# Kernel optimization log

Measured on AMD Instinct MI355X. Metric: run time of the kernel, lower is better.

The kernel has to match this reference:

```python
import jax, jax.numpy as jnp
import numpy as np

B = 32          # batch_size (scenes)
P_PER_B = 256   # proposals per scene (max_n_proposals, equal by construction)
N = B * P_PER_B # total proposals = 8192
PTS = 1024      # points per proposal
M = 128         # cfg.m, instance feature dim
LANG = 256      # lang_size
H = 128         # hidden_size
EPS = 1e-5      # BatchNorm eps


def setup_inputs() -> dict:
    key = jax.random.key(0)
    ks = jax.random.split(key, 16)
    feats = jax.random.normal(ks[0], (N, M), jnp.float32)
    total_pts = N * PTS
    # proposals_idx: (total_pts, 2) = [proposal_id, global_point_id]; points are
    # contiguous per proposal, proposals contiguous per scene.
    prop_ids = jnp.repeat(jnp.arange(N, dtype=jnp.int32), PTS)
    pt_ids = jnp.arange(total_pts, dtype=jnp.int32)
    proposals_idx = jnp.stack([prop_ids, pt_ids], axis=1)
    proposals_offset = jnp.arange(N + 1, dtype=jnp.int32) * PTS
    b_offsets = jnp.arange(B + 1, dtype=jnp.int32) * (P_PER_B * PTS)
    lang_emb = jax.random.normal(ks[1], (B, LANG), jnp.float32)
    # parameters: fuse = Conv1d(LANG+M -> H, k=1) + ReLU
    W_fuse = jax.random.normal(ks[2], (H, LANG + M), jnp.float32) * 0.05
    b_fuse = jnp.zeros((H,), jnp.float32)
    # match = Conv1d(H,H,1)+ReLU+BN, Conv1d(H,H,1)+ReLU+BN, Conv1d(H,1,1)
    W1 = jax.random.normal(ks[3], (H, H), jnp.float32) * 0.05
    b1 = jnp.zeros((H,), jnp.float32)
    g1 = jnp.ones((H,), jnp.float32)
    be1 = jnp.zeros((H,), jnp.float32)
    rm1 = jax.random.normal(ks[4], (H,), jnp.float32) * 0.1
    rv1 = jax.random.uniform(ks[5], (H,), jnp.float32, 0.5, 1.5)
    W2 = jax.random.normal(ks[6], (H, H), jnp.float32) * 0.05
    b2 = jnp.zeros((H,), jnp.float32)
    g2 = jnp.ones((H,), jnp.float32)
    be2 = jnp.zeros((H,), jnp.float32)
    rm2 = jax.random.normal(ks[7], (H,), jnp.float32) * 0.1
    rv2 = jax.random.uniform(ks[8], (H,), jnp.float32, 0.5, 1.5)
    W3 = jax.random.normal(ks[9], (1, H), jnp.float32) * 0.05
    b3 = jnp.zeros((1,), jnp.float32)
    return {
        'aggregated_vote_features': feats,
        'proposals_idx': proposals_idx,
        'proposals_offset': proposals_offset,
        'b_offsets': b_offsets,
        'lang_emb': lang_emb,
        'W_fuse': W_fuse, 'b_fuse': b_fuse,
        'W1': W1, 'b1': b1, 'g1': g1, 'be1': be1, 'rm1': rm1, 'rv1': rv1,
        'W2': W2, 'b2': b2, 'g2': g2, 'be2': be2, 'rm2': rm2, 'rv2': rv2,
        'W3': W3, 'b3': b3,
    }


def _bn(x, g, be, rm, rv):
    # eval-mode BatchNorm1d over channel dim of (B, C, P)
    scale = g / jnp.sqrt(rv + EPS)
    return (x - rm[None, :, None]) * scale[None, :, None] + be[None, :, None]


def reference(aggregated_vote_features, proposals_idx, proposals_offset, b_offsets,
              lang_emb, W_fuse, b_fuse, W1, b1, g1, be1, rm1, rv1,
              W2, b2, g2, be2, rm2, rv2, W3, b3):
    # --- vectorized replacement of the host-sync batch-id loop ---
    first_pts = proposals_idx[proposals_offset[:-1], 1]            # (N,) first point of each proposal
    bid = jnp.searchsorted(b_offsets, first_pts, side='right') - 1  # (N,) proposal_batch_ids
    # --- ragged -> padded gather (vectorized scatter by per-batch position) ---
    counts = jax.ops.segment_sum(jnp.ones_like(bid), bid, num_segments=B)
    offs = jnp.concatenate([jnp.zeros((1,), counts.dtype), jnp.cumsum(counts)[:-1]])
    order = jnp.argsort(bid)                                       # stable sort keeps original order per batch
    bid_s = bid[order]
    pos = jnp.arange(bid.shape[0]) - offs[bid_s]                   # position within its batch
    padded = jnp.zeros((B, P_PER_B, M), aggregated_vote_features.dtype)
    padded = padded.at[bid_s, pos].set(aggregated_vote_features[order])  # (B, P, M)
    # --- concat language features and run 1x1 conv chain ---
    lang = jnp.broadcast_to(lang_emb[:, None, :], (B, P_PER_B, LANG))
    x = jnp.concatenate([padded, lang], axis=-1)                   # (B, P, M+LANG)
    x = jnp.einsum('bpc,oc->bop', x, W_fuse) + b_fuse[None, :, None]
    x = jax.nn.relu(x)                                             # fuse
    x = _bn(jax.nn.relu(jnp.einsum('bcp,oc->bop', x, W1) + b1[None, :, None]), g1, be1, rm1, rv1)
    x = _bn(jax.nn.relu(jnp.einsum('bcp,oc->bop', x, W2) + b2[None, :, None]), g2, be2, rm2, rv2)
    conf = jnp.einsum('bcp,oc->bop', x, W3) + b3[None, :, None]    # (B, 1, P)
    return conf[:, 0, :]                                           # cluster_ref: (B, P)
```

## Files before the change

### kernel.cpp

```cpp
#include <hip/hip_runtime.h>
#include <math.h>

#define B_    32
#define PPB   256
#define N_    (B_*PPB)
#define M_    128
#define LANG_ 256
#define H_    128
#define EPS_  1e-5f
#define MC    16

typedef __attribute__((ext_vector_type(8))) short s16x8;
typedef __attribute__((ext_vector_type(4))) float f32x4;

static __device__ __forceinline__ unsigned short f2bf(float x) {
  unsigned int u = __float_as_uint(x);
  unsigned int r = (u + 0x7fff + ((u >> 16) & 1)) >> 16;
  return (unsigned short)r;
}
static __device__ __forceinline__ float bf2f(unsigned short h) {
  return __uint_as_float(((unsigned int)h) << 16);
}

__global__ __launch_bounds__(256) void k_prep(
    const int* __restrict__ pidx, const int* __restrict__ poff,
    int* __restrict__ fp_c,
    const float* __restrict__ Wf, const float* __restrict__ lang,
    float* __restrict__ lp,
    const float* __restrict__ W1, const float* __restrict__ W2,
    unsigned short* __restrict__ wa)
{
  const int tid = threadIdx.x;
  const int lane = tid & 63, wid = tid >> 6;
  const int o16 = lane & 15, g = lane >> 4;
  const int i = blockIdx.x * 256 + tid;

  const int off = poff[i];
  fp_c[i] = pidx[2 * off + 1];

  {
    const int o = tid >> 1, hf = tid & 1;
    float acc = 0.f;
    const int l0 = hf * 128;
    #pragma unroll 8
    for (int l = l0; l < l0 + 128; l += 4) {
      const float4 w = *reinterpret_cast<const float4*>(Wf + o * 384 + 128 + l);
      const float4 e = *reinterpret_cast<const float4*>(lang + blockIdx.x * LANG_ + l);
      acc += w.x * e.x + w.y * e.y + w.z * e.z + w.w * e.w;
    }
    acc += __shfl_xor(acc, 1);
    if (hf == 0) lp[blockIdx.x * H_ + o] = acc;
  }

  for (int G = blockIdx.x * 4 + wid; G < 192; G += 128) {
    const int L = G >> 6, s = (G >> 3) & 7, t = G & 7;
    const float* Wsrc; int str;
    if (L == 0)      { Wsrc = Wf; str = 384; }
    else if (L == 1) { Wsrc = W1; str = H_; }
    else             { Wsrc = W2; str = H_; }
    const int o = t * 16 + o16, sp = s & 3;
    const bool hi = (s < 4);
    const float* rowp = Wsrc + (size_t)o * str + sp * 32 + g * 4;
    const float4 a = *reinterpret_cast<const float4*>(rowp);
    const float4 bq = *reinterpret_cast<const float4*>(rowp + 16);
    const float av[8] = {a.x, a.y, a.z, a.w, bq.x, bq.y, bq.z, bq.w};
    s16x8 v;
    #pragma unroll
    for (int e = 0; e < 8; ++e) {
      const unsigned short h = f2bf(av[e]);
      v[e] = (short)(hi ? h : f2bf(av[e] - bf2f(h)));
    }
    *reinterpret_cast<s16x8*>(wa + (size_t)G * 512 + lane * 8) = v;
  }
}

#define MFMA_LAYER(Aarr)                                                     \
  {                                                                          \
    _Pragma("unroll")                                                        \
    for (int sg = 0; sg < 8; ++sg) {                                         \
      const s16x8 bb = (sg < 4) ? Bh[sg] : Bl[sg - 4];                       \
      acc[0] = __builtin_amdgcn_mfma_f32_16x16x32_bf16(Aarr[0][sg], bb, acc[0], 0, 0, 0); \
      acc[1] = __builtin_amdgcn_mfma_f32_16x16x32_bf16(Aarr[1][sg], bb, acc[1], 0, 0, 0); \
    }                                                                        \
    _Pragma("unroll")                                                        \
    for (int sg = 0; sg < 8; ++sg) {                                         \
      const s16x8 bb = (sg < 4) ? Bl[sg] : Bh[sg - 4];                       \
      acc[0] = __builtin_amdgcn_mfma_f32_16x16x32_bf16(Aarr[0][sg], bb, acc[0], 0, 0, 0); \
      acc[1] = __builtin_amdgcn_mfma_f32_16x16x32_bf16(Aarr[1][sg], bb, acc[1], 0, 0, 0); \
    }                                                                        \
  }

#define READ_B()                                                             \
  {                                                                          \
    _Pragma("unroll")                                                        \
    for (int s = 0; s < 4; ++s) {                                            \
      const int idx = (s * 4 + g) * 16 + o16;                                \
      Bh[s] = XbHi[idx];                                                     \
      Bl[s] = XbLo[idx];                                                     \
    }                                                                        \
  }

#define LOAD_A(Aarr, LL)                                                     \
  {                                                                          \
    _Pragma("unroll")                                                        \
    for (int t = 0; t < 2; ++t)                                              \
      _Pragma("unroll")                                                      \
      for (int s = 0; s < 8; ++s)                                            \
        Aarr[t][s] = *reinterpret_cast<const s16x8*>(                        \
            wa + (size_t)(((LL) * 8 + s) * 8 + (wid * 2 + t)) * 512 + lane * 8); \
  }

__global__ __launch_bounds__(256, 2) void k_mlp(
    const float* __restrict__ feats,
    const unsigned short* __restrict__ wa,
    const int* __restrict__ fp_c, const int* __restrict__ boff,
    const float* __restrict__ bf, const float* __restrict__ b1,
    const float* __restrict__ g1, const float* __restrict__ be1,
    const float* __restrict__ rm1, const float* __restrict__ rv1,
    const float* __restrict__ b2, const float* __restrict__ g2,
    const float* __restrict__ be2, const float* __restrict__ rm2,
    const float* __restrict__ rv2,
    const float* __restrict__ W3, const float* __restrict__ b3,
    const float* __restrict__ lpg,
    float* __restrict__ out)
{
  __shared__ s16x8 XbHi[256];
  __shared__ s16x8 XbLo[256];
  __shared__ float pbuf[1024];
  __shared__ float outp[64];
  __shared__ int   sSrow[MC];
  __shared__ int   wtot[4];

  const int tid = threadIdx.x;
  const int lane = tid & 63, wid = tid >> 6;
  const int o16 = lane & 15, g = lane >> 4;
  const int q0 = blockIdx.x * MC;
  const int b = q0 >> 8;
  const int r0 = q0 & 255;

  if (tid < MC) sSrow[tid] = -1;
  const int blo = boff[b], bhi = boff[b + 1];
  const int i0 = tid * 32;
  unsigned mask = 0u;
  #pragma unroll
  for (int jj = 0; jj < 8; ++jj) {
    const int4 pv = *reinterpret_cast<const int4*>(fp_c + i0 + jj * 4);
    const int fps[4] = {pv.x, pv.y, pv.z, pv.w};
    #pragma unroll
    for (int e = 0; e < 4; ++e)
      mask |= (fps[e] >= blo && fps[e] < bhi) ? (1u << (jj * 4 + e)) : 0u;
  }
  const int cnt = __popc(mask);
  int sc = cnt;
  #pragma unroll
  for (int d = 1; d < 64; d <<= 1) {
    const int v = __shfl_up(sc, d);
    if (lane >= d) sc += v;
  }
  if (lane == 63) wtot[wid] = sc;
  __syncthreads();
  int base = sc - cnt;
  #pragma unroll
  for (int w = 0; w < 4; ++w) if (w < wid) base += wtot[w];
  {
    unsigned m = mask;
    int r = base;
    while (m) {
      const int j = __ffs(m) - 1;
      if (r >= r0 && r < r0 + MC) sSrow[r - r0] = i0 + j;
      ++r;
      m &= m - 1;
    }
  }

  s16x8 A0[2][8], A1[2][8], A2[2][8];
  LOAD_A(A0, 0);

  #pragma unroll
  for (int j = tid; j < 1024; j += 256) {
    const int arr = j >> 7, o = j & 127;
    float v;
    switch (arr) {
      case 0: v = bf[o] + lpg[b * H_ + o]; break;
      case 1: v = b1[o]; break;
      case 2: v = g1[o] * rsqrtf(rv1[o] + EPS_); break;
      case 3: { const float s = g1[o] * rsqrtf(rv1[o] + EPS_);
                v = be1[o] - rm1[o] * s; } break;
      case 4: v = b2[o]; break;
      case 5: v = g2[o] * rsqrtf(rv2[o] + EPS_); break;
      case 6: { const float s = g2[o] * rsqrtf(rv2[o] + EPS_);
                v = be2[o] - rm2[o] * s; } break;
      default: v = W3[o]; break;
    }
    pbuf[j] = v;
  }
  __syncthreads();

  {
    const int n = tid & 15, u = tid >> 4;
    const int s = u >> 2, gg = u & 3;
    const int srow = sSrow[n];
    const int k0 = s * 32 + gg * 4;
    float4 a = make_float4(0.f, 0.f, 0.f, 0.f), bq = a;
    if (srow >= 0) {
      a  = *reinterpret_cast<const float4*>(feats + (size_t)srow * M_ + k0);
      bq = *reinterpret_cast<const float4*>(feats + (size_t)srow * M_ + k0 + 16);
    }
    const float av[8] = {a.x, a.y, a.z, a.w, bq.x, bq.y, bq.z, bq.w};
    s16x8 hv, lv;
    #pragma unroll
    for (int e = 0; e < 8; ++e) {
      const unsigned short h = f2bf(av[e]);
      hv[e] = (short)h;
      lv[e] = (short)f2bf(av[e] - bf2f(h));
    }
    XbHi[u * 16 + n] = hv;
    XbLo[u * 16 + n] = lv;
  }
  __syncthreads();

  f32x4 acc[2];
  s16x8 Bh[4], Bl[4];

  READ_B();
  __syncthreads();
  LOAD_A(A1, 1);
  acc[0] = (f32x4){0.f, 0.f, 0.f, 0.f};
  acc[1] = (f32x4){0.f, 0.f, 0.f, 0.f};
  MFMA_LAYER(A0);
  {
    s16x8 hv, lv;
    #pragma unroll
    for (int t = 0; t < 2; ++t)
      #pragma unroll
      for (int r = 0; r < 4; ++r) {
        const int o = (wid * 2 + t) * 16 + g * 4 + r;
        const float v = fmaxf(acc[t][r] + pbuf[o], 0.f);
        const unsigned short h = f2bf(v);
        hv[t * 4 + r] = (short)h;
        lv[t * 4 + r] = (short)f2bf(v - bf2f(h));
      }
    const int widx = (wid * 4 + g) * 16 + o16;
    XbHi[widx] = hv;
    XbLo[widx] = lv;
  }
  __syncthreads();

  READ_B();
  __syncthreads();
  LOAD_A(A2, 2);
  acc[0] = (f32x4){0.f, 0.f, 0.f, 0.f};
  acc[1] = (f32x4){0.f, 0.f, 0.f, 0.f};
  MFMA_LAYER(A1);
  {
    s16x8 hv, lv;
    #pragma unroll
    for (int t = 0; t < 2; ++t)
      #pragma unroll
      for (int r = 0; r < 4; ++r) {
        const int o = (wid * 2 + t) * 16 + g * 4 + r;
        const float v = fmaxf(acc[t][r] + pbuf[128 + o], 0.f) * pbuf[256 + o]
                        + pbuf[384 + o];
        const unsigned short h = f2bf(v);
        hv[t * 4 + r] = (short)h;
        lv[t * 4 + r] = (short)f2bf(v - bf2f(h));
      }
    const int widx = (wid * 4 + g) * 16 + o16;
    XbHi[widx] = hv;
    XbLo[widx] = lv;
  }
  __syncthreads();

  READ_B();
  acc[0] = (f32x4){0.f, 0.f, 0.f, 0.f};
  acc[1] = (f32x4){0.f, 0.f, 0.f, 0.f};
  MFMA_LAYER(A2);
  {
    float p0 = 0.f;
    #pragma unroll
    for (int t = 0; t < 2; ++t)
      #pragma unroll
      for (int r = 0; r < 4; ++r) {
        const int o = (wid * 2 + t) * 16 + g * 4 + r;
        p0 += pbuf[896 + o] *
              (fmaxf(acc[t][r] + pbuf[512 + o], 0.f) * pbuf[640 + o] + pbuf[768 + o]);
      }
    p0 += __shfl_xor(p0, 16);
    p0 += __shfl_xor(p0, 32);
    if (lane < 16) outp[wid * 16 + lane] = p0;
    __syncthreads();
    if (tid < 16)
      out[q0 + tid] = outp[tid] + outp[16 + tid] + outp[32 + tid] + outp[48 + tid] + b3[0];
  }
}

extern "C" void kernel_launch(void* const* d_in, const int* in_sizes, int n_in,
                              void* d_out, int out_size, void* d_ws, size_t ws_size,
                              hipStream_t stream) {
  const float* feats = (const float*)d_in[0];
  const int*   pidx  = (const int*)d_in[1];
  const int*   poff  = (const int*)d_in[2];
  const int*   boff  = (const int*)d_in[3];
  const float* lang  = (const float*)d_in[4];
  const float* Wf    = (const float*)d_in[5];
  const float* bf    = (const float*)d_in[6];
  const float* W1    = (const float*)d_in[7];
  const float* b1    = (const float*)d_in[8];
  const float* g1    = (const float*)d_in[9];
  const float* be1   = (const float*)d_in[10];
  const float* rm1   = (const float*)d_in[11];
  const float* rv1   = (const float*)d_in[12];
  const float* W2    = (const float*)d_in[13];
  const float* b2    = (const float*)d_in[14];
  const float* g2    = (const float*)d_in[15];
  const float* be2   = (const float*)d_in[16];
  const float* rm2   = (const float*)d_in[17];
  const float* rv2   = (const float*)d_in[18];
  const float* W3    = (const float*)d_in[19];
  const float* b3    = (const float*)d_in[20];
  float* out = (float*)d_out;

  int*            fp_c = (int*)d_ws;
  float*          lp   = (float*)((char*)d_ws + 32768);
  unsigned short* wa   = (unsigned short*)((char*)d_ws + 49152);

  hipLaunchKernelGGL(k_prep, dim3(32), dim3(256), 0, stream,
                     pidx, poff, fp_c, Wf, lang, lp, W1, W2, wa);
  hipLaunchKernelGGL(k_mlp, dim3(N_ / MC), dim3(256), 0, stream,
                     feats, wa, fp_c, boff, bf, b1, g1, be1, rm1, rv1,
                     b2, g2, be2, rm2, rv2, W3, b3, lp, out);
}
```

Baseline: 23.31 us.

## Process 32 proposals per block with 8 waves, each wave owning one output tile

Each block now handles 32 proposals with 512 threads. Every wave holds one 16-row slice of the weight matrices instead of two, and reuses each A fragment across two 16-column proposal tiles. The per-block weight loads from global memory are amortized over twice as many proposals and the grid is halved. Activations are written to LDS as packed 64-bit stores. In exchange each thread scans half as many proposal ids, but block-level barriers now cover twice as many waves.

```diff
diff --git a/kernel.cpp b/kernel.cpp
--- a/kernel.cpp
+++ b/kernel.cpp
@@ -8,10 +8,12 @@
 #define LANG_ 256
 #define H_    128
 #define EPS_  1e-5f
-#define MC    16
+#define MC    32
+#define NBLK  (N_/MC)
 
 typedef __attribute__((ext_vector_type(8))) short s16x8;
 typedef __attribute__((ext_vector_type(4))) float f32x4;
+typedef unsigned long long ull_t;
 
 static __device__ __forceinline__ unsigned short f2bf(float x) {
   unsigned int u = __float_as_uint(x);
@@ -74,43 +76,66 @@
   }
 }
 
+#define LOAD_A(Aarr, LL)                                                     \
+  {                                                                          \
+    _Pragma("unroll")                                                        \
+    for (int s = 0; s < 8; ++s)                                              \
+      Aarr[s] = *reinterpret_cast<const s16x8*>(                             \
+          wa + (size_t)(((LL) * 8 + s) * 8 + wid) * 512 + lane * 8);         \
+  }
+
+#define READ_B()                                                             \
+  {                                                                          \
+    _Pragma("unroll")                                                        \
+    for (int s = 0; s < 4; ++s)                                              \
+      _Pragma("unroll")                                                      \
+      for (int nt = 0; nt < 2; ++nt) {                                       \
+        const int idx = (s * 4 + g) * 32 + nt * 16 + o16;                    \
+        Bh[s][nt] = XbHi[idx];                                               \
+        Bl[s][nt] = XbLo[idx];                                               \
+      }                                                                      \
+  }
+
 #define MFMA_LAYER(Aarr)                                                     \
   {                                                                          \
     _Pragma("unroll")                                                        \
-    for (int sg = 0; sg < 8; ++sg) {                                         \
-      const s16x8 bb = (sg < 4) ? Bh[sg] : Bl[sg - 4];                       \
-      acc[0] = __builtin_amdgcn_mfma_f32_16x16x32_bf16(Aarr[0][sg], bb, acc[0], 0, 0, 0); \
-      acc[1] = __builtin_amdgcn_mfma_f32_16x16x32_bf16(Aarr[1][sg], bb, acc[1], 0, 0, 0); \
+    for (int sg = 0; sg < 8; ++sg)                                           \
+      _Pragma("unroll")                                                      \
+      for (int nt = 0; nt < 2; ++nt) {                                       \
+        const s16x8 bb = (sg < 4) ? Bh[sg][nt] : Bl[sg - 4][nt];             \
+        acc[nt] = __builtin_amdgcn_mfma_f32_16x16x32_bf16(Aarr[sg], bb, acc[nt], 0, 0, 0); \
+      }                                                                      \
+    _Pragma("unroll")                                                        \
+    for (int sg = 0; sg < 8; ++sg)                                           \
+      _Pragma("unroll")                                                      \
+      for (int nt = 0; nt < 2; ++nt) {                                       \
+        const s16x8 bb = (sg < 4) ? Bl[sg][nt] : Bh[sg - 4][nt];             \
+        acc[nt] = __builtin_amdgcn_mfma_f32_16x16x32_bf16(Aarr[sg], bb, acc[nt], 0, 0, 0); \
+      }                                                                      \
+  }
+
+#define ACT_STORE(EXPR_V)                                                    \
+  {                                                                          \
+    _Pragma("unroll")                                                        \
+    for (int nt = 0; nt < 2; ++nt) {                                         \
+      ull_t hv64 = 0, lv64 = 0;                                              \
+      _Pragma("unroll")                                                      \
+      for (int r = 0; r < 4; ++r) {                                          \
+        const int o = wid * 16 + g * 4 + r;                                  \
+        const float z = acc[nt][r];                                          \
+        const float v = (EXPR_V);                                            \
+        const unsigned short h = f2bf(v);                                    \
+        const unsigned short l = f2bf(v - bf2f(h));                          \
+        hv64 |= (ull_t)h << (16 * r);                                        \
+        lv64 |= (ull_t)l << (16 * r);                                        \
+      }                                                                      \
+      const int f = ((wid >> 1) * 4 + g) * 32 + nt * 16 + o16;               \
+      reinterpret_cast<ull_t*>(XbHi)[f * 2 + (wid & 1)] = hv64;              \
+      reinterpret_cast<ull_t*>(XbLo)[f * 2 + (wid & 1)] = lv64;              \
     }                                                                        \
-    _Pragma("unroll")                                                        \
-    for (int sg = 0; sg < 8; ++sg) {                                         \
-      const s16x8 bb = (sg < 4) ? Bl[sg] : Bh[sg - 4];                       \
-      acc[0] = __builtin_amdgcn_mfma_f32_16x16x32_bf16(Aarr[0][sg], bb, acc[0], 0, 0, 0); \
-      acc[1] = __builtin_amdgcn_mfma_f32_16x16x32_bf16(Aarr[1][sg], bb, acc[1], 0, 0, 0); \
-    }                                                                        \
-  }
-
-#define READ_B()                                                             \
-  {                                                                          \
-    _Pragma("unroll")                                                        \
-    for (int s = 0; s < 4; ++s) {                                            \
-      const int idx = (s * 4 + g) * 16 + o16;                                \
-      Bh[s] = XbHi[idx];                                                     \
-      Bl[s] = XbLo[idx];                                                     \
-    }                                                                        \
-  }
-
-#define LOAD_A(Aarr, LL)                                                     \
-  {                                                                          \
-    _Pragma("unroll")                                                        \
-    for (int t = 0; t < 2; ++t)                                              \
-      _Pragma("unroll")                                                      \
-      for (int s = 0; s < 8; ++s)                                            \
-        Aarr[t][s] = *reinterpret_cast<const s16x8*>(                        \
-            wa + (size_t)(((LL) * 8 + s) * 8 + (wid * 2 + t)) * 512 + lane * 8); \
-  }
-
-__global__ __launch_bounds__(256, 2) void k_mlp(
+  }
+
+__global__ __launch_bounds__(512, 2) void k_mlp(
     const float* __restrict__ feats,
     const unsigned short* __restrict__ wa,
     const int* __restrict__ fp_c, const int* __restrict__ boff,
@@ -124,12 +149,12 @@
     const float* __restrict__ lpg,
     float* __restrict__ out)
 {
-  __shared__ s16x8 XbHi[256];
-  __shared__ s16x8 XbLo[256];
+  __shared__ s16x8 XbHi[512];
+  __shared__ s16x8 XbLo[512];
   __shared__ float pbuf[1024];
-  __shared__ float outp[64];
+  __shared__ float outp[8][32];
   __shared__ int   sSrow[MC];
-  __shared__ int   wtot[4];
+  __shared__ int   wtot[8];
 
   const int tid = threadIdx.x;
   const int lane = tid & 63, wid = tid >> 6;
@@ -140,10 +165,10 @@
 
   if (tid < MC) sSrow[tid] = -1;
   const int blo = boff[b], bhi = boff[b + 1];
-  const int i0 = tid * 32;
+  const int i0 = tid * 16;
   unsigned mask = 0u;
   #pragma unroll
-  for (int jj = 0; jj < 8; ++jj) {
+  for (int jj = 0; jj < 4; ++jj) {
     const int4 pv = *reinterpret_cast<const int4*>(fp_c + i0 + jj * 4);
     const int fps[4] = {pv.x, pv.y, pv.z, pv.w};
     #pragma unroll
@@ -161,7 +186,7 @@
   __syncthreads();
   int base = sc - cnt;
   #pragma unroll
-  for (int w = 0; w < 4; ++w) if (w < wid) base += wtot[w];
+  for (int w = 0; w < 8; ++w) if (w < wid) base += wtot[w];
   {
     unsigned m = mask;
     int r = base;
@@ -173,11 +198,11 @@
     }
   }
 
-  s16x8 A0[2][8], A1[2][8], A2[2][8];
+  s16x8 A0[8], A1[8], A2[8];
   LOAD_A(A0, 0);
 
   #pragma unroll
-  for (int j = tid; j < 1024; j += 256) {
+  for (int j = tid; j < 1024; j += 512) {
     const int arr = j >> 7, o = j & 127;
     float v;
     switch (arr) {
@@ -197,7 +222,7 @@
   __syncthreads();
 
   {
-    const int n = tid & 15, u = tid >> 4;
+    const int n = tid & 31, u = tid >> 5;
     const int s = u >> 2, gg = u & 3;
     const int srow = sSrow[n];
     const int k0 = s * 32 + gg * 4;
@@ -214,13 +239,13 @@
       hv[e] = (short)h;
       lv[e] = (short)f2bf(av[e] - bf2f(h));
     }
-    XbHi[u * 16 + n] = hv;
-    XbLo[u * 16 + n] = lv;
+    XbHi[u * 32 + n] = hv;
+    XbLo[u * 32 + n] = lv;
   }
   __syncthreads();
 
   f32x4 acc[2];
-  s16x8 Bh[4], Bl[4];
+  s16x8 Bh[4][2], Bl[4][2];
 
   READ_B();
   __syncthreads();
@@ -228,22 +253,7 @@
   acc[0] = (f32x4){0.f, 0.f, 0.f, 0.f};
   acc[1] = (f32x4){0.f, 0.f, 0.f, 0.f};
   MFMA_LAYER(A0);
-  {
-    s16x8 hv, lv;
-    #pragma unroll
-    for (int t = 0; t < 2; ++t)
-      #pragma unroll
-      for (int r = 0; r < 4; ++r) {
-        const int o = (wid * 2 + t) * 16 + g * 4 + r;
-        const float v = fmaxf(acc[t][r] + pbuf[o], 0.f);
-        const unsigned short h = f2bf(v);
-        hv[t * 4 + r] = (short)h;
-        lv[t * 4 + r] = (short)f2bf(v - bf2f(h));
-      }
-    const int widx = (wid * 4 + g) * 16 + o16;
-    XbHi[widx] = hv;
-    XbLo[widx] = lv;
-  }
+  ACT_STORE(fmaxf(z + pbuf[o], 0.f));
   __syncthreads();
 
   READ_B();
@@ -252,23 +262,7 @@
   acc[0] = (f32x4){0.f, 0.f, 0.f, 0.f};
   acc[1] = (f32x4){0.f, 0.f, 0.f, 0.f};
   MFMA_LAYER(A1);
-  {
-    s16x8 hv, lv;
-    #pragma unroll
-    for (int t = 0; t < 2; ++t)
-      #pragma unroll
-      for (int r = 0; r < 4; ++r) {
-        const int o = (wid * 2 + t) * 16 + g * 4 + r;
-        const float v = fmaxf(acc[t][r] + pbuf[128 + o], 0.f) * pbuf[256 + o]
-                        + pbuf[384 + o];
-        const unsigned short h = f2bf(v);
-        hv[t * 4 + r] = (short)h;
-        lv[t * 4 + r] = (short)f2bf(v - bf2f(h));
-      }
-    const int widx = (wid * 4 + g) * 16 + o16;
-    XbHi[widx] = hv;
-    XbLo[widx] = lv;
-  }
+  ACT_STORE(fmaxf(z + pbuf[128 + o], 0.f) * pbuf[256 + o] + pbuf[384 + o]);
   __syncthreads();
 
   READ_B();
@@ -276,21 +270,28 @@
   acc[1] = (f32x4){0.f, 0.f, 0.f, 0.f};
   MFMA_LAYER(A2);
   {
-    float p0 = 0.f;
+    float p0 = 0.f, p1 = 0.f;
     #pragma unroll
-    for (int t = 0; t < 2; ++t)
+    for (int r = 0; r < 4; ++r) {
+      const int o = wid * 16 + g * 4 + r;
+      const float w3 = pbuf[896 + o];
+      const float bb2 = pbuf[512 + o], ss2 = pbuf[640 + o], tt2 = pbuf[768 + o];
+      p0 += w3 * (fmaxf(acc[0][r] + bb2, 0.f) * ss2 + tt2);
+      p1 += w3 * (fmaxf(acc[1][r] + bb2, 0.f) * ss2 + tt2);
+    }
+    p0 += __shfl_xor(p0, 16); p0 += __shfl_xor(p0, 32);
+    p1 += __shfl_xor(p1, 16); p1 += __shfl_xor(p1, 32);
+    if (lane < 16) {
+      outp[wid][o16] = p0;
+      outp[wid][16 + o16] = p1;
+    }
+    __syncthreads();
+    if (tid < 32) {
+      float s = b3[0];
       #pragma unroll
-      for (int r = 0; r < 4; ++r) {
-        const int o = (wid * 2 + t) * 16 + g * 4 + r;
-        p0 += pbuf[896 + o] *
-              (fmaxf(acc[t][r] + pbuf[512 + o], 0.f) * pbuf[640 + o] + pbuf[768 + o]);
-      }
-    p0 += __shfl_xor(p0, 16);
-    p0 += __shfl_xor(p0, 32);
-    if (lane < 16) outp[wid * 16 + lane] = p0;
-    __syncthreads();
-    if (tid < 16)
-      out[q0 + tid] = outp[tid] + outp[16 + tid] + outp[32 + tid] + outp[48 + tid] + b3[0];
+      for (int w = 0; w < 8; ++w) s += outp[w][tid];
+      out[q0 + tid] = s;
+    }
   }
 }
 
@@ -326,7 +327,7 @@
 
   hipLaunchKernelGGL(k_prep, dim3(32), dim3(256), 0, stream,
                      pidx, poff, fp_c, Wf, lang, lp, W1, W2, wa);
-  hipLaunchKernelGGL(k_mlp, dim3(N_ / MC), dim3(256), 0, stream,
+  hipLaunchKernelGGL(k_mlp, dim3(NBLK), dim3(512), 0, stream,
                      feats, wa, fp_c, boff, bf, b1, g1, be1, rm1, rv1,
                      b2, g2, be2, rm2, rv2, W3, b3, lp, out);
 }
```

Result: faster. 21.39 us (-8.2%).
